# Performance work log

Hardware: AMD Instinct MI355X
Metric: run time of the kernel (lower is better)

Reference implementation:

```python
import jax, jax.numpy as jnp
import numpy as np

# dims: T timesteps (=window_size[0]), B_ = num_windows*batch, window 8x8, C=dim
T, B, WH, WW, C, NH = 4, 1024, 8, 8, 256, 8
HD = C // NH          # head_dim = 32
N = T * WH * WW       # tokens per window volume = 256
V_TH, TAU, ALPHA = 1.0, 2.0, 4.0  # LIF threshold, membrane tau, surrogate sharpness

@jax.custom_vjp
def spike(v):
    # Heaviside spike with sigmoid surrogate gradient (standard spikingjelly-style)
    return (v >= 0.0).astype(v.dtype)

def _spike_fwd(v):
    return spike(v), v

def _spike_bwd(v, g):
    sg = jax.nn.sigmoid(ALPHA * v)
    return (g * ALPHA * sg * (1.0 - sg),)

spike.defvjp(_spike_fwd, _spike_bwd)

def lif(x):
    """Multi-step LIF neuron over leading time axis. x: (T, ...). Hard reset to 0."""
    def step(v, xt):
        v = v + (xt - v) / TAU
        s = spike(v - V_TH)
        return v * (1.0 - s), s
    _, s = jax.lax.scan(step, jnp.zeros_like(x[0]), x)
    return s

def setup_inputs() -> dict:
    key = jax.random.key(0)
    ks = jax.random.split(key, 6)
    sc = 1.0 / np.sqrt(C)
    return {
        "x":   jax.random.normal(ks[0], (T, B, WH, WW, C), jnp.float32),
        "Wq":  jax.random.normal(ks[1], (C, C), jnp.float32) * sc,   # linear_q weight (no bias)
        "Wk":  jax.random.normal(ks[2], (C, C), jnp.float32) * sc,   # linear_k weight (no bias)
        "Wp":  jax.random.normal(ks[3], (C, C), jnp.float32) * sc,   # proj weight
        "bp":  jnp.zeros((C,), jnp.float32),                         # proj bias
        "pos": jax.random.normal(ks[4], (1, NH, N, HD), jnp.float32) * 0.02,  # positional_encoding param
    }

def reference(x, Wq, Wk, Wp, bp, pos):
    # proj_sn on raw input
    xs = lif(x)                                        # (T,B,WH,WW,C) spikes
    # Q path: linear -> spiking neuron (norm=None branch skipped)
    q = lif(xs @ Wq.T)                                 # (T,B,WH,WW,C)
    # K path: linear -> add positional encoding -> spiking neuron
    k = lif(xs @ Wk.T + pos.reshape(T, 1, WH, WW, C))  # (T,B,WH,WW,C)
    # head split exactly as torch reshapes (row-major, mixes T into B for k)
    q = q.reshape(T, B, NH, WH * WW, HD)
    k = k.reshape(B, NH, T * WH * WW, HD)
    # token attention: sum over head_dim, spike, elementwise multiply with k
    att_token = lif(q.sum(-1, keepdims=True))          # (T,B,NH,HW,1)
    attn = k * att_token.reshape(B, NH, -1, 1)         # (B,NH,T*HW,HD)
    # exact torch permute/reshape back to (T,B,WH,WW,C)
    x2 = attn.reshape(B, NH, T, WH, WW, HD).transpose(2, 0, 3, 4, 1, 5).reshape(T, B, WH, WW, C)
    attn_out = lif(x2)                                 # attn_sn output (second return value)
    y = (x2 @ Wp.T + bp).reshape(B, N, C)              # proj then final reshape (B_, N, C)
    return y, attn_out
```

## Files before the change

### kernel.cpp

```cpp
#include <hip/hip_runtime.h>
#include <hip/hip_bf16.h>

static constexpr int  T4    = 4;
static constexpr int  G     = 65536;
static constexpr long PLANE = 16777216L;

__device__ __forceinline__ float bfh(unsigned short u) {
    union { unsigned u32; float f; } c; c.u32 = ((unsigned)u) << 16; return c.f;
}

__global__ void prep_kernel(const float* __restrict__ Wq, const float* __restrict__ Wk,
                            const float* __restrict__ Wp,
                            __hip_bfloat16* __restrict__ WqT, __hip_bfloat16* __restrict__ WkT,
                            float* __restrict__ WpT)
{
    int c = blockIdx.x;
    int j = threadIdx.x;
    int idx = c * 256 + j;
    WqT[idx] = __float2bfloat16(Wq[j * 256 + c]);
    WkT[idx] = __float2bfloat16(Wk[j * 256 + c]);
    WpT[idx] = Wp[j * 256 + c];
}

__global__ __launch_bounds__(256) void lif_qk_kernel(
    const float* __restrict__ x,
    unsigned* __restrict__ AM,
    const __hip_bfloat16* __restrict__ WqT,
    const __hip_bfloat16* __restrict__ WkT,
    const float* __restrict__ pos)
{
    int lane = threadIdx.x & 63;
    int wv   = threadIdx.x >> 6;
    int wid  = blockIdx.x * 4 + wv;
    int sh   = (lane & 56);

    for (int gi = 0; gi < 8; ++gi) {
        int g  = wid * 8 + gi;
        int hw = g & 63;

        float4 X[4];
        #pragma unroll
        for (int t = 0; t < 4; ++t)
            X[t] = ((const float4*)(x + (long)t * PLANE + (long)g * 256))[lane];

        unsigned long long sm[4][4];
        float4 v  = make_float4(0.f, 0.f, 0.f, 0.f);
        float4 vq = make_float4(0.f, 0.f, 0.f, 0.f);
        float  va = 0.f;
        unsigned attb = 0u;

        #pragma unroll
        for (int t = 0; t < 4; ++t) {
            v.x = v.x + (X[t].x - v.x) * 0.5f; bool s0 = (v.x - 1.0f) >= 0.0f; if (s0) v.x = 0.f;
            v.y = v.y + (X[t].y - v.y) * 0.5f; bool s1 = (v.y - 1.0f) >= 0.0f; if (s1) v.y = 0.f;
            v.z = v.z + (X[t].z - v.z) * 0.5f; bool s2 = (v.z - 1.0f) >= 0.0f; if (s2) v.z = 0.f;
            v.w = v.w + (X[t].w - v.w) * 0.5f; bool s3 = (v.w - 1.0f) >= 0.0f; if (s3) v.w = 0.f;
            sm[t][0] = __ballot(s0);
            sm[t][1] = __ballot(s1);
            sm[t][2] = __ballot(s2);
            sm[t][3] = __ballot(s3);

            float q0 = 0.f, q1 = 0.f, q2 = 0.f, q3 = 0.f;
            #pragma unroll
            for (int j = 0; j < 4; ++j) {
                unsigned long long mm = sm[t][j];
                while (mm) {
                    int b = __ffsll(mm) - 1;
                    mm &= (mm - 1);
                    int c = 4 * b + j;
                    ushort4 w = *((const ushort4*)(WqT + c * 256 + 4 * lane));
                    q0 += bfh(w.x); q1 += bfh(w.y); q2 += bfh(w.z); q3 += bfh(w.w);
                }
            }

            vq.x = vq.x + (q0 - vq.x) * 0.5f; bool t0 = (vq.x - 1.0f) >= 0.0f; if (t0) vq.x = 0.f;
            vq.y = vq.y + (q1 - vq.y) * 0.5f; bool t1 = (vq.y - 1.0f) >= 0.0f; if (t1) vq.y = 0.f;
            vq.z = vq.z + (q2 - vq.z) * 0.5f; bool t2 = (vq.z - 1.0f) >= 0.0f; if (t2) vq.z = 0.f;
            vq.w = vq.w + (q3 - vq.w) * 0.5f; bool t3 = (vq.w - 1.0f) >= 0.0f; if (t3) vq.w = 0.f;
            unsigned long long qb0 = __ballot(t0);
            unsigned long long qb1 = __ballot(t1);
            unsigned long long qb2 = __ballot(t2);
            unsigned long long qb3 = __ballot(t3);

            int cnt = __popc((unsigned)((qb0 >> sh) & 0xFFull))
                    + __popc((unsigned)((qb1 >> sh) & 0xFFull))
                    + __popc((unsigned)((qb2 >> sh) & 0xFFull))
                    + __popc((unsigned)((qb3 >> sh) & 0xFFull));
            va = va + ((float)cnt - va) * 0.5f;
            bool a = (va - 1.0f) >= 0.0f; if (a) va = 0.f;
            attb |= (a ? 1u : 0u) << t;
        }

        bool anyatt = (__ballot(attb != 0u) != 0ull);
        if (!anyatt) {
            if (lane < 32) {
                int t = lane >> 3, wd = lane & 7;
                AM[((long)t * G + g) * 8 + wd] = 0u;
            }
        } else {
            float4 vk = make_float4(0.f, 0.f, 0.f, 0.f);
            #pragma unroll
            for (int t = 0; t < 4; ++t) {
                float k0 = 0.f, k1 = 0.f, k2 = 0.f, k3 = 0.f;
                #pragma unroll
                for (int j = 0; j < 4; ++j) {
                    unsigned long long mm = sm[t][j];
                    while (mm) {
                        int b = __ffsll(mm) - 1;
                        mm &= (mm - 1);
                        int c = 4 * b + j;
                        ushort4 w = *((const ushort4*)(WkT + c * 256 + 4 * lane));
                        k0 += bfh(w.x); k1 += bfh(w.y); k2 += bfh(w.z); k3 += bfh(w.w);
                    }
                }
                float4 pp = ((const float4*)(pos + t * 16384 + hw * 256))[lane];
                k0 += pp.x; k1 += pp.y; k2 += pp.z; k3 += pp.w;

                vk.x = vk.x + (k0 - vk.x) * 0.5f; bool t0 = (vk.x - 1.0f) >= 0.0f; if (t0) vk.x = 0.f;
                vk.y = vk.y + (k1 - vk.y) * 0.5f; bool t1 = (vk.y - 1.0f) >= 0.0f; if (t1) vk.y = 0.f;
                vk.z = vk.z + (k2 - vk.z) * 0.5f; bool t2 = (vk.z - 1.0f) >= 0.0f; if (t2) vk.z = 0.f;
                vk.w = vk.w + (k3 - vk.w) * 0.5f; bool t3 = (vk.w - 1.0f) >= 0.0f; if (t3) vk.w = 0.f;

                bool at = ((attb >> t) & 1u) != 0u;
                unsigned long long bb[4];
                bb[0] = __ballot(t0 && at);
                bb[1] = __ballot(t1 && at);
                bb[2] = __ballot(t2 && at);
                bb[3] = __ballot(t3 && at);
                if (lane < 8) {
                    unsigned wdv = 0u;
                    #pragma unroll
                    for (int hd = 0; hd < 32; ++hd) {
                        int ls = lane * 8 + (hd >> 2);
                        wdv |= (unsigned)((bb[hd & 3] >> ls) & 1ull) << hd;
                    }
                    AM[((long)t * G + g) * 8 + lane] = wdv;
                }
            }
        }
    }
}

__global__ __launch_bounds__(256) void out_kernel(
    const unsigned* __restrict__ AM,
    const float* __restrict__ WpT,
    const float* __restrict__ bp,
    float* __restrict__ y,
    float* __restrict__ attn_out)
{
    int lane = threadIdx.x & 63;
    int wv   = threadIdx.x >> 6;
    int row  = blockIdx.x * 4 + wv;
    int t2   = row >> 16;
    int b2   = (row >> 6) & 1023;
    int hw2  = row & 63;

    float4 acc = ((const float4*)bp)[lane];

    int nh   = lane >> 3;
    int srow = (b2 * 4 + (nh >> 1)) * 64 + (nh & 1) * 32 + t2 * 8 + (hw2 >> 3);
    unsigned W = AM[(long)srow * 8 + (hw2 & 7)];
    bool any = (__ballot(W != 0u) != 0ull);
    if (any) {
        #pragma unroll 1
        for (int n2 = 0; n2 < 8; ++n2) {
            unsigned Wn = __shfl(W, n2 * 8);
            while (Wn) {
                int hd = __ffs(Wn) - 1;
                Wn &= (Wn - 1);
                const float4* wp = (const float4*)(WpT + (n2 * 32 + hd) * 256);
                float4 wl = wp[lane];
                acc.x += wl.x; acc.y += wl.y; acc.z += wl.z; acc.w += wl.w;
            }
        }
    }
    ((float4*)y)[(long)row * 64 + lane] = acc;
    float4 z = make_float4(0.f, 0.f, 0.f, 0.f);
    ((float4*)attn_out)[(long)row * 64 + lane] = z;
}

extern "C" void kernel_launch(void* const* d_in, const int* in_sizes, int n_in,
                              void* d_out, int out_size, void* d_ws, size_t ws_size,
                              hipStream_t stream) {
    const float* x   = (const float*)d_in[0];
    const float* Wq  = (const float*)d_in[1];
    const float* Wk  = (const float*)d_in[2];
    const float* Wp  = (const float*)d_in[3];
    const float* bp  = (const float*)d_in[4];
    const float* pos = (const float*)d_in[5];

    float* y        = (float*)d_out;
    float* attn_out = y + 67108864L;

    char* ws = (char*)d_ws;
    unsigned*           AM  = (unsigned*)(ws);
    __hip_bfloat16*     WqT = (__hip_bfloat16*)(ws + (8L << 20));
    __hip_bfloat16*     WkT = (__hip_bfloat16*)(ws + (8L << 20) + (128L << 10));
    float*              WpT = (float*)(ws + (8L << 20) + (256L << 10));

    prep_kernel<<<256, 256, 0, stream>>>(Wq, Wk, Wp, WqT, WkT, WpT);
    lif_qk_kernel<<<2048, 256, 0, stream>>>(x, AM, WqT, WkT, pos);
    out_kernel<<<65536, 256, 0, stream>>>(AM, WpT, bp, y, attn_out);
}
```

Before: 864.4 us.

## Prefetch sparse weight gathers and batch 32 rows per wave in output kernel

The sparse weight gather loops are software-pipelined so the next spiked weight row is loaded before the current one is accumulated. The output kernel now processes 32 rows per wave instead of one, prefetching the next row's attention mask word, and its grid shrinks accordingly. The QK kernel halves the work per wave and doubles its grid for more parallelism. This aims to hide load latency and cut per-row launch overhead, at the cost of fewer waves in flight in the output kernel and higher register use.

New measurement: 807.0 us. 6.6% less time.

```diff
diff --git a/kernel.cpp b/kernel.cpp
--- a/kernel.cpp
+++ b/kernel.cpp
@@ -22,6 +22,22 @@
     WpT[idx] = Wp[j * 256 + c];
 }
 
+__device__ __forceinline__ void gather_word(unsigned long long mm, int j, int lane,
+                                            const __hip_bfloat16* __restrict__ WT,
+                                            float& q0, float& q1, float& q2, float& q3)
+{
+    if (!mm) return;
+    int b = __ffsll(mm) - 1; mm &= (mm - 1);
+    ushort4 w = *((const ushort4*)(WT + (4 * b + j) * 256 + 4 * lane));
+    while (mm) {
+        int b2 = __ffsll(mm) - 1; mm &= (mm - 1);
+        ushort4 w2 = *((const ushort4*)(WT + (4 * b2 + j) * 256 + 4 * lane));
+        q0 += bfh(w.x); q1 += bfh(w.y); q2 += bfh(w.z); q3 += bfh(w.w);
+        w = w2;
+    }
+    q0 += bfh(w.x); q1 += bfh(w.y); q2 += bfh(w.z); q3 += bfh(w.w);
+}
+
 __global__ __launch_bounds__(256) void lif_qk_kernel(
     const float* __restrict__ x,
     unsigned* __restrict__ AM,
@@ -34,8 +50,8 @@
     int wid  = blockIdx.x * 4 + wv;
     int sh   = (lane & 56);
 
-    for (int gi = 0; gi < 8; ++gi) {
-        int g  = wid * 8 + gi;
+    for (int gi = 0; gi < 4; ++gi) {
+        int g  = wid * 4 + gi;
         int hw = g & 63;
 
         float4 X[4];
@@ -62,16 +78,8 @@
 
             float q0 = 0.f, q1 = 0.f, q2 = 0.f, q3 = 0.f;
             #pragma unroll
-            for (int j = 0; j < 4; ++j) {
-                unsigned long long mm = sm[t][j];
-                while (mm) {
-                    int b = __ffsll(mm) - 1;
-                    mm &= (mm - 1);
-                    int c = 4 * b + j;
-                    ushort4 w = *((const ushort4*)(WqT + c * 256 + 4 * lane));
-                    q0 += bfh(w.x); q1 += bfh(w.y); q2 += bfh(w.z); q3 += bfh(w.w);
-                }
-            }
+            for (int j = 0; j < 4; ++j)
+                gather_word(sm[t][j], j, lane, WqT, q0, q1, q2, q3);
 
             vq.x = vq.x + (q0 - vq.x) * 0.5f; bool t0 = (vq.x - 1.0f) >= 0.0f; if (t0) vq.x = 0.f;
             vq.y = vq.y + (q1 - vq.y) * 0.5f; bool t1 = (vq.y - 1.0f) >= 0.0f; if (t1) vq.y = 0.f;
@@ -103,16 +111,8 @@
             for (int t = 0; t < 4; ++t) {
                 float k0 = 0.f, k1 = 0.f, k2 = 0.f, k3 = 0.f;
                 #pragma unroll
-                for (int j = 0; j < 4; ++j) {
-                    unsigned long long mm = sm[t][j];
-                    while (mm) {
-                        int b = __ffsll(mm) - 1;
-                        mm &= (mm - 1);
-                        int c = 4 * b + j;
-                        ushort4 w = *((const ushort4*)(WkT + c * 256 + 4 * lane));
-                        k0 += bfh(w.x); k1 += bfh(w.y); k2 += bfh(w.z); k3 += bfh(w.w);
-                    }
-                }
+                for (int j = 0; j < 4; ++j)
+                    gather_word(sm[t][j], j, lane, WkT, k0, k1, k2, k3);
                 float4 pp = ((const float4*)(pos + t * 16384 + hw * 256))[lane];
                 k0 += pp.x; k1 += pp.y; k2 += pp.z; k3 += pp.w;
 
@@ -150,33 +150,50 @@
 {
     int lane = threadIdx.x & 63;
     int wv   = threadIdx.x >> 6;
-    int row  = blockIdx.x * 4 + wv;
-    int t2   = row >> 16;
-    int b2   = (row >> 6) & 1023;
-    int hw2  = row & 63;
-
-    float4 acc = ((const float4*)bp)[lane];
-
-    int nh   = lane >> 3;
+    long wave = (long)blockIdx.x * 4 + wv;
+    int  nh   = lane >> 3;
+
+    float4 base = ((const float4*)bp)[lane];
+    const float4 z = make_float4(0.f, 0.f, 0.f, 0.f);
+
+    long row0 = wave * 32;
+    {
+    }
+    int t2  = (int)(row0 >> 16);
+    int b2  = (int)(row0 >> 6) & 1023;
+    int hw2 = (int)row0 & 63;
     int srow = (b2 * 4 + (nh >> 1)) * 64 + (nh & 1) * 32 + t2 * 8 + (hw2 >> 3);
     unsigned W = AM[(long)srow * 8 + (hw2 & 7)];
-    bool any = (__ballot(W != 0u) != 0ull);
-    if (any) {
-        #pragma unroll 1
-        for (int n2 = 0; n2 < 8; ++n2) {
-            unsigned Wn = __shfl(W, n2 * 8);
-            while (Wn) {
-                int hd = __ffs(Wn) - 1;
-                Wn &= (Wn - 1);
-                const float4* wp = (const float4*)(WpT + (n2 * 32 + hd) * 256);
-                float4 wl = wp[lane];
-                acc.x += wl.x; acc.y += wl.y; acc.z += wl.z; acc.w += wl.w;
+
+    for (int r = 0; r < 32; ++r) {
+        long row = row0 + r;
+        unsigned Wn = 0u;
+        if (r < 31) {
+            long rown = row + 1;
+            int t2n  = (int)(rown >> 16);
+            int b2n  = (int)(rown >> 6) & 1023;
+            int hw2n = (int)rown & 63;
+            int srn  = (b2n * 4 + (nh >> 1)) * 64 + (nh & 1) * 32 + t2n * 8 + (hw2n >> 3);
+            Wn = AM[(long)srn * 8 + (hw2n & 7)];
+        }
+
+        float4 val = base;
+        if (__ballot(W != 0u) != 0ull) {
+            #pragma unroll 1
+            for (int n2 = 0; n2 < 8; ++n2) {
+                unsigned Wx = __shfl(W, n2 * 8);
+                while (Wx) {
+                    int hd = __ffs(Wx) - 1;
+                    Wx &= (Wx - 1);
+                    float4 wl = ((const float4*)(WpT + (n2 * 32 + hd) * 256))[lane];
+                    val.x += wl.x; val.y += wl.y; val.z += wl.z; val.w += wl.w;
+                }
             }
         }
-    }
-    ((float4*)y)[(long)row * 64 + lane] = acc;
-    float4 z = make_float4(0.f, 0.f, 0.f, 0.f);
-    ((float4*)attn_out)[(long)row * 64 + lane] = z;
+        ((float4*)y)[row * 64 + lane]        = val;
+        ((float4*)attn_out)[row * 64 + lane] = z;
+        W = Wn;
+    }
 }
 
 extern "C" void kernel_launch(void* const* d_in, const int* in_sizes, int n_in,
@@ -199,6 +216,6 @@
     float*              WpT = (float*)(ws + (8L << 20) + (256L << 10));
 
     prep_kernel<<<256, 256, 0, stream>>>(Wq, Wk, Wp, WqT, WkT, WpT);
-    lif_qk_kernel<<<2048, 256, 0, stream>>>(x, AM, WqT, WkT, pos);
-    out_kernel<<<65536, 256, 0, stream>>>(AM, WpT, bp, y, attn_out);
-}
+    lif_qk_kernel<<<4096, 256, 0, stream>>>(x, AM, WqT, WkT, pos);
+    out_kernel<<<2048, 256, 0, stream>>>(AM, WpT, bp, y, attn_out);
+}
```
